# Kernel tuning notes

Measured on AMD Instinct MI355X. Metric: run time of the kernel, lower is better.

Reference implementation:

```python
import jax, jax.numpy as jnp
import numpy as np

B, T, N, E, H, L, K = 2, 32, 256, 1024, 16, 2, 256
MAXLEN = 512  # RelativeMultiheadAttention max_seq_len default
SCALES = (1, 2, 4)
TAU = 1.0


def setup_inputs() -> dict:
    key = jax.random.key(0)
    ks = jax.random.split(key, 9)
    s = 0.02
    A = 2 * L  # [layer0-spatial, layer0-temporal, layer1-spatial, layer1-temporal]
    return {
        "x": jax.random.normal(ks[0], (B, T, N, E), jnp.float32),
        "attn_wq": jax.random.normal(ks[1], (A, E, E), jnp.float32) * s,
        "attn_bq": jnp.zeros((A, E), jnp.float32),
        "attn_wk": jax.random.normal(ks[2], (A, E, E), jnp.float32) * s,
        "attn_bk": jnp.zeros((A, E), jnp.float32),
        "attn_wv": jax.random.normal(ks[3], (A, E, E), jnp.float32) * s,
        "attn_bv": jnp.zeros((A, E), jnp.float32),
        "attn_wd": jax.random.normal(ks[4], (A, E, E), jnp.float32) * s,
        "attn_bd": jnp.zeros((A, E), jnp.float32),
        "rel_bias": jax.random.normal(ks[5], (A, 2 * MAXLEN - 1, H), jnp.float32) * s,
        "sel_w": jax.random.normal(ks[6], (E, K), jnp.float32) * s,
        "sel_b": jnp.zeros((K,), jnp.float32),
    }


def _rel_attn(x, wq, bq, wk, bk, wv, bv, wd, bd, rb):
    # x: [Bx, S, E]; rb: [2*MAXLEN-1, H]
    Bx, S, _ = x.shape
    D = E // H
    q = (x @ wq + bq).reshape(Bx, S, H, D)
    k = (x @ wk + bk).reshape(Bx, S, H, D)
    v = (x @ wv + bv).reshape(Bx, S, H, D)
    scores = jnp.einsum('bshd,bthd->bhst', q, k) / jnp.sqrt(jnp.asarray(D, x.dtype))
    pos = jnp.arange(S)
    idx = pos[None, :] - pos[:, None] + (MAXLEN - 1)  # [S, S]
    bias = rb[idx]  # [S, S, H] gathered relative-position bias
    scores = scores + bias.transpose(2, 0, 1)[None]
    w = jax.nn.softmax(scores, axis=-1)
    ctx = jnp.einsum('bhst,bthd->bshd', w, v).reshape(Bx, S, E)
    return ctx @ wd + bd


def reference(x, attn_wq, attn_bq, attn_wk, attn_bk, attn_wv, attn_bv,
              attn_wd, attn_bd, rel_bias, sel_w, sel_b):
    h = x
    for l in range(L):
        # spatial attention over tokens within each frame
        i = 2 * l
        hs = h.reshape(B * T, N, E)
        hs = _rel_attn(hs, attn_wq[i], attn_bq[i], attn_wk[i], attn_bk[i],
                       attn_wv[i], attn_bv[i], attn_wd[i], attn_bd[i], rel_bias[i])
        # temporal attention across frames per spatial location
        j = 2 * l + 1
        ht = hs.reshape(B, T, N, E).transpose(0, 2, 1, 3).reshape(B * N, T, E)
        ht = _rel_attn(ht, attn_wq[j], attn_bq[j], attn_wk[j], attn_bk[j],
                       attn_wv[j], attn_bv[j], attn_wd[j], attn_bd[j], rel_bias[j])
        h = ht.reshape(B, N, T, E).transpose(0, 2, 1, 3)
    # DifferentiableTokenSelection: softmax-weighted pooling into K tokens
    flat = h.reshape(B, T * N, E)
    sc = flat @ sel_w + sel_b  # [B, T*N, K]
    wts = jax.nn.softmax(sc / TAU, axis=1)
    sel = jnp.einsum('bmk,bme->bke', wts, flat)  # [B, K, E]
    # multi-scale average pooling (kernel==stride==scale), concat along tokens
    outs = [sel.reshape(B, K // s, s, E).mean(axis=2) for s in SCALES]
    return jnp.concatenate(outs, axis=1)  # [B, K + K//2 + K//4, E]
```

## Files before the change

kernel.cpp:

```cpp
#include <hip/hip_runtime.h>
#include <stdint.h>


using f16x8 = __attribute__((ext_vector_type(8))) _Float16;
using f16x4 = __attribute__((ext_vector_type(4))) _Float16;
using f32x4 = __attribute__((ext_vector_type(4))) float;

__device__ __forceinline__ int tmap_dev(int m) {
    int bx = m >> 5;
    int s  = m & 31;
    int b  = bx >> 8;
    int n  = bx & 255;
    return (((b << 5) + s) << 8) + n;
}

__device__ __forceinline__ void load16(const _Float16* g, _Float16* l)
{
    __builtin_amdgcn_global_load_lds(
        (const __attribute__((address_space(1))) unsigned int*)g,
        (__attribute__((address_space(3))) unsigned int*)l,
        16, 0, 0);
}

__device__ __forceinline__ void split_f16(float v, _Float16& h, _Float16& l)
{
    h = (_Float16)v;
    l = (_Float16)(v - (float)h);
}

__global__ __launch_bounds__(256)
void conv_act(const float* __restrict__ src, _Float16* __restrict__ dh,
              _Float16* __restrict__ dl, int m_off)
{
    int idx = blockIdx.x * 256 + threadIdx.x;
    int e = idx << 3;
    int ml = e >> 10, col = e & 1023;
    const float* s = src + (size_t)(m_off + ml) * 1024 + col;
    float4 a = *(const float4*)s;
    float4 b = *(const float4*)(s + 4);
    float vv[8] = {a.x, a.y, a.z, a.w, b.x, b.y, b.z, b.w};
    f16x8 vh, vl;
    #pragma unroll
    for (int r = 0; r < 8; r++) {
        _Float16 h, l;
        split_f16(vv[r], h, l);
        vh[r] = h; vl[r] = l;
    }
    *(f16x8*)(dh + (size_t)ml * 1024 + col) = vh;
    *(f16x8*)(dl + (size_t)ml * 1024 + col) = vl;
}

__global__ __launch_bounds__(256)
void conv_wT(const float* __restrict__ W, _Float16* __restrict__ Th,
             _Float16* __restrict__ Tl, int ncols)
{
    __shared__ float Ls[64][65];
    const int n0 = blockIdx.x * 64, k0 = blockIdx.y * 64;
    const int t = threadIdx.x;
    const int kk = t >> 4, nn = (t & 15) << 2;
    #pragma unroll
    for (int i = 0; i < 4; i++) {
        float4 v = *(const float4*)(W + (size_t)(k0 + kk + 16 * i) * ncols + n0 + nn);
        Ls[kk + 16 * i][nn + 0] = v.x; Ls[kk + 16 * i][nn + 1] = v.y;
        Ls[kk + 16 * i][nn + 2] = v.z; Ls[kk + 16 * i][nn + 3] = v.w;
    }
    __syncthreads();
    const int nl = t >> 4, kc = (t & 15) << 2;
    #pragma unroll
    for (int i = 0; i < 4; i++) {
        int n = nl + 16 * i;
        f16x4 hh, ll;
        #pragma unroll
        for (int c = 0; c < 4; c++) {
            _Float16 h, l;
            split_f16(Ls[kc + c][n], h, l);
            hh[c] = h; ll[c] = l;
        }
        *(f16x4*)(Th + (size_t)(n0 + n) * 1024 + k0 + kc) = hh;
        *(f16x4*)(Tl + (size_t)(n0 + n) * 1024 + k0 + kc) = ll;
    }
}

template<int EPI>
__device__ __forceinline__ void gemm_core(
    const _Float16* __restrict__ Ah, const _Float16* __restrict__ Al,
    const _Float16* __restrict__ Wh, const _Float16* __restrict__ Wl,
    const float* __restrict__ bias,
    float* __restrict__ C, _Float16* __restrict__ Ch, _Float16* __restrict__ Cl,
    int ldc, int map_in, int m_off_in, int map_out, int m_off_out,
    int n0, int m0)
{
    __shared__ uint32_t smem_u[8512];
    _Float16* smem = (_Float16*)smem_u;
    _Float16* sAh = smem;
    _Float16* sAl = smem + 4096;
    _Float16* sBh = smem + 8192;
    _Float16* sBl = smem + 12288;

    const int tid = threadIdx.x;
    const int lane = tid & 63;
    const int wv = tid >> 6;
    const int fm = (wv >> 1) << 6;
    const int fn = (wv & 1) << 6;
    const int lm = lane & 15, lq = lane >> 4;

    f32x4 acc[4][4] = {};

    const int srow = tid >> 2;
    const int skc  = (tid & 3) << 3;
    const int gm0 = m_off_in + m0 + srow;
    const int gm1 = gm0 + 64;
    const int r0 = map_in ? tmap_dev(gm0) : gm0;
    const int r1 = map_in ? tmap_dev(gm1) : gm1;
    const _Float16* gAh0 = Ah + (size_t)r0 * 1024 + skc;
    const _Float16* gAh1 = Ah + (size_t)r1 * 1024 + skc;
    const _Float16* gAl0 = Al + (size_t)r0 * 1024 + skc;
    const _Float16* gAl1 = Al + (size_t)r1 * 1024 + skc;
    const _Float16* gB0 = Wh + (size_t)(n0 + srow) * 1024 + skc;
    const _Float16* gB1 = Wl + (size_t)(n0 + srow) * 1024 + skc;
    const int lo = tid << 3;

    for (int k0 = 0; k0 < 1024; k0 += 32) {
        load16(gAh0 + k0, sAh + lo);
        load16(gAh1 + k0, sAh + lo + 2048);
        load16(gAl0 + k0, sAl + lo);
        load16(gAl1 + k0, sAl + lo + 2048);
        load16(gB0 + k0,         sBh + lo);
        load16(gB0 + k0 + 65536, sBh + lo + 2048);
        load16(gB1 + k0,         sBl + lo);
        load16(gB1 + k0 + 65536, sBl + lo + 2048);
        __syncthreads();

        f16x8 ah[4], al[4], bh[4], bl[4];
        #pragma unroll
        for (int i = 0; i < 4; i++) {
            int ra = (fm + i * 16 + lm) * 32 + lq * 8;
            ah[i] = *(const f16x8*)(sAh + ra);
            al[i] = *(const f16x8*)(sAl + ra);
            int rb_ = (fn + i * 16 + lm) * 32 + lq * 8;
            bh[i] = *(const f16x8*)(sBh + rb_);
            bl[i] = *(const f16x8*)(sBl + rb_);
        }
        #pragma unroll
        for (int i = 0; i < 4; i++)
            #pragma unroll
            for (int j = 0; j < 4; j++) {
                acc[i][j] = __builtin_amdgcn_mfma_f32_16x16x32_f16(ah[i], bh[j], acc[i][j], 0, 0, 0);
                acc[i][j] = __builtin_amdgcn_mfma_f32_16x16x32_f16(ah[i], bl[j], acc[i][j], 0, 0, 0);
                acc[i][j] = __builtin_amdgcn_mfma_f32_16x16x32_f16(al[i], bh[j], acc[i][j], 0, 0, 0);
            }
        __syncthreads();
    }

    if (EPI == 0) {
        #pragma unroll
        for (int j = 0; j < 4; j++) {
            int n = n0 + fn + j * 16 + lm;
            float bb = bias[n];
            #pragma unroll
            for (int i = 0; i < 4; i++) {
                #pragma unroll
                for (int r = 0; r < 4; r++) {
                    int gm = m_off_out + m0 + fm + i * 16 + lq * 4 + r;
                    int row = map_out ? tmap_dev(gm) : gm;
                    C[(size_t)row * ldc + n] = acc[i][j][r] + bb;
                }
            }
        }
    }
}

__global__ __launch_bounds__(256, 2)
void gemm_f16s_f32(const _Float16* __restrict__ Ah, const _Float16* __restrict__ Al,
                   int map_in, int m_off_in,
                   const _Float16* __restrict__ Wh, const _Float16* __restrict__ Wl,
                   const float* __restrict__ bias, float* __restrict__ C, int ldc,
                   int map_out, int m_off_out)
{
    gemm_core<0>(Ah, Al, Wh, Wl, bias, C, nullptr, nullptr, ldc,
                 map_in, m_off_in, map_out, m_off_out,
                 blockIdx.x * 128, blockIdx.y * 128);
}

template<int EPI>
__device__ __forceinline__ void gemm256_core(
    uint32_t* __restrict__ smem_u,
    const _Float16* __restrict__ Ah, const _Float16* __restrict__ Al,
    const _Float16* __restrict__ Wh, const _Float16* __restrict__ Wl,
    const float* __restrict__ bias,
    _Float16* __restrict__ Ch, _Float16* __restrict__ Cl,
    int map_in, int m_off_in, int map_out, int m_off_out,
    int n0, int m0)
{
    _Float16* S = (_Float16*)smem_u;
    const int tid  = threadIdx.x;
    const int lane = tid & 63;
    const int wv = tid >> 6;
    const int wm = wv >> 1;
    const int fm = wm << 6;
    const int fn = (wv & 1) << 6;
    const int lm = lane & 15, lq = lane >> 4;
    const int ko = ((lq ^ ((lm >> 1) & 3)) << 3);

    f32x4 acc[4][4] = {};

    const int srow = tid >> 2;
    const int scol = (((tid & 3) ^ ((tid >> 3) & 3)) << 3);
    const int gm0 = m_off_in + m0 + srow;
    const int gm1 = gm0 + 128;
    const int r0 = map_in ? tmap_dev(gm0) : gm0;
    const int r1 = map_in ? tmap_dev(gm1) : gm1;
    const _Float16* gAh0 = Ah + (size_t)r0 * 1024 + scol;
    const _Float16* gAh1 = Ah + (size_t)r1 * 1024 + scol;
    const _Float16* gAl0 = Al + (size_t)r0 * 1024 + scol;
    const _Float16* gAl1 = Al + (size_t)r1 * 1024 + scol;
    const _Float16* gBh  = Wh + (size_t)(n0 + srow) * 1024 + scol;
    const _Float16* gBl  = Wl + (size_t)(n0 + srow) * 1024 + scol;
    const int lo = tid << 3;

    auto stage = [&](int t, int b) {
        const int k0 = t << 5;
        _Float16* d = S + b * 24576;
        load16(gAh0 + k0, d + lo);
        load16(gAh1 + k0, d + 4096  + lo);
        load16(gAl0 + k0, d + 8192  + lo);
        load16(gAl1 + k0, d + 12288 + lo);
        load16(gBh  + k0, d + 16384 + lo);
        load16(gBl  + k0, d + 20480 + lo);
    };

    auto ldfrags = [&](const _Float16* c,
                       f16x8 (&xah)[4], f16x8 (&xal)[4],
                       f16x8 (&xbh)[4], f16x8 (&xbl)[4]) {
        #pragma unroll
        for (int i = 0; i < 4; i++) {
            int ra = (fm + i * 16 + lm) * 32 + ko;
            xah[i] = *(const f16x8*)(c + ra);
            xal[i] = *(const f16x8*)(c + 8192 + ra);
            int rb = (fn + i * 16 + lm) * 32 + ko;
            xbh[i] = *(const f16x8*)(c + 16384 + rb);
            xbl[i] = *(const f16x8*)(c + 20480 + rb);
        }
    };

    f16x8 ahA[4], alA[4], bhA[4], blA[4];
    f16x8 ahB[4], alB[4], bhB[4], blB[4];

    auto kstep = [&](int t, int nxtbuf, int stagebuf,
                     f16x8 (&cah)[4], f16x8 (&cal)[4],
                     f16x8 (&cbh)[4], f16x8 (&cbl)[4],
                     f16x8 (&nah)[4], f16x8 (&nal)[4],
                     f16x8 (&nbh)[4], f16x8 (&nbl)[4],
                     bool prefetch, bool dostage) {
        if (prefetch) ldfrags(S + nxtbuf * 24576, nah, nal, nbh, nbl);
        if (dostage) stage(t + 2, stagebuf);
        __builtin_amdgcn_sched_barrier(0);
        __builtin_amdgcn_s_setprio(1);
        #pragma unroll
        for (int i = 0; i < 4; i++)
            #pragma unroll
            for (int j = 0; j < 4; j++) {
                acc[i][j] = __builtin_amdgcn_mfma_f32_16x16x32_f16(cah[i], cbh[j], acc[i][j], 0, 0, 0);
                acc[i][j] = __builtin_amdgcn_mfma_f32_16x16x32_f16(cah[i], cbl[j], acc[i][j], 0, 0, 0);
                acc[i][j] = __builtin_amdgcn_mfma_f32_16x16x32_f16(cal[i], cbh[j], acc[i][j], 0, 0, 0);
            }
        __builtin_amdgcn_s_setprio(0);
        asm volatile("s_waitcnt vmcnt(0)" ::: "memory");
        __builtin_amdgcn_s_barrier();
    };

    stage(0, 0);
    stage(1, 1);
    asm volatile("s_waitcnt vmcnt(0)" ::: "memory");
    __builtin_amdgcn_s_barrier();
    ldfrags(S, ahA, alA, bhA, blA);

    #pragma unroll 1
    for (int tt = 0; tt < 30; tt += 6) {
        kstep(tt + 0, 1, 2, ahA, alA, bhA, blA, ahB, alB, bhB, blB, true, true);
        kstep(tt + 1, 2, 0, ahB, alB, bhB, blB, ahA, alA, bhA, blA, true, true);
        kstep(tt + 2, 0, 1, ahA, alA, bhA, blA, ahB, alB, bhB, blB, true, true);
        kstep(tt + 3, 1, 2, ahB, alB, bhB, blB, ahA, alA, bhA, blA, true, true);
        kstep(tt + 4, 2, 0, ahA, alA, bhA, blA, ahB, alB, bhB, blB, true, true);
        kstep(tt + 5, 0, 1, ahB, alB, bhB, blB, ahA, alA, bhA, blA, true, true);
    }
    kstep(30, 1, 0, ahA, alA, bhA, blA, ahB, alB, bhB, blB, true,  false);
    kstep(31, 0, 0, ahB, alB, bhB, blB, ahA, alA, bhA, blA, false, false);

    if (EPI == 1) {
        #pragma unroll 1
        for (int q = 0; q < 4; q++) {
            __syncthreads();
            if (wm == q) {
                #pragma unroll
                for (int j = 0; j < 4; j++) {
                    int ncol = fn + j * 16 + lm;
                    float bb = bias[n0 + ncol];
                    #pragma unroll
                    for (int i = 0; i < 4; i++) {
                        #pragma unroll
                        for (int r = 0; r < 4; r++) {
                            float v = acc[i][j][r] + bb;
                            _Float16 h, l;
                            split_f16(v, h, l);
                            uint32_t ph = (uint32_t)__builtin_bit_cast(unsigned short, h);
                            uint32_t pl = (uint32_t)__builtin_bit_cast(unsigned short, l);
                            smem_u[(i * 16 + lq * 4 + r) * 132 + ncol] = ph | (pl << 16);
                        }
                    }
                }
            }
            __syncthreads();
            #pragma unroll
            for (int g = 0; g < 2; g++) {
                int u = tid + g * 512;
                int rl = u >> 4;
                int c8 = (u & 15) << 3;
                uint32_t p[8];
                #pragma unroll
                for (int x = 0; x < 8; x++) p[x] = smem_u[rl * 132 + c8 + x];
                f16x8 hh, ll;
                #pragma unroll
                for (int x = 0; x < 8; x++) {
                    hh[x] = __builtin_bit_cast(_Float16, (unsigned short)(p[x] & 0xffff));
                    ll[x] = __builtin_bit_cast(_Float16, (unsigned short)(p[x] >> 16));
                }
                int gm = m_off_out + m0 + q * 64 + rl;
                int row = map_out ? tmap_dev(gm) : gm;
                *(f16x8*)(Ch + (size_t)row * 1024 + n0 + c8) = hh;
                *(f16x8*)(Cl + (size_t)row * 1024 + n0 + c8) = ll;
            }
        }
    } else {
        #pragma unroll 1
        for (int q = 0; q < 4; q++) {
            __syncthreads();
            if (wm == q) {
                #pragma unroll
                for (int j = 0; j < 4; j++) {
                    int ncol = fn + j * 16 + lm;
                    float bb = bias[n0 + ncol];
                    #pragma unroll
                    for (int i = 0; i < 4; i++) {
                        #pragma unroll
                        for (int r = 0; r < 4; r++) {
                            float v = acc[i][j][r] + bb;
                            _Float16 h, l;
                            split_f16(v, h, l);
                            uint32_t ph = (uint32_t)__builtin_bit_cast(unsigned short, h);
                            uint32_t pl = (uint32_t)__builtin_bit_cast(unsigned short, l);
                            smem_u[(i * 16 + lq * 4 + r) * 129 + ncol] = ph | (pl << 16);
                        }
                    }
                }
            }
            __syncthreads();
            #pragma unroll
            for (int g = 0; g < 4; g++) {
                int u = tid + g * 512;
                int nn = u >> 4;
                int mg = (u & 15) << 2;
                uint32_t p0 = smem_u[(mg + 0) * 129 + nn];
                uint32_t p1 = smem_u[(mg + 1) * 129 + nn];
                uint32_t p2 = smem_u[(mg + 2) * 129 + nn];
                uint32_t p3 = smem_u[(mg + 3) * 129 + nn];
                f16x4 hh, ll;
                hh[0] = __builtin_bit_cast(_Float16, (unsigned short)(p0 & 0xffff));
                hh[1] = __builtin_bit_cast(_Float16, (unsigned short)(p1 & 0xffff));
                hh[2] = __builtin_bit_cast(_Float16, (unsigned short)(p2 & 0xffff));
                hh[3] = __builtin_bit_cast(_Float16, (unsigned short)(p3 & 0xffff));
                ll[0] = __builtin_bit_cast(_Float16, (unsigned short)(p0 >> 16));
                ll[1] = __builtin_bit_cast(_Float16, (unsigned short)(p1 >> 16));
                ll[2] = __builtin_bit_cast(_Float16, (unsigned short)(p2 >> 16));
                ll[3] = __builtin_bit_cast(_Float16, (unsigned short)(p3 >> 16));
                size_t off = (size_t)(n0 + nn) * 8192 + (m0 + q * 64 + mg);
                *(f16x4*)(Ch + off) = hh;
                *(f16x4*)(Cl + off) = ll;
            }
        }
    }
}

__global__ __launch_bounds__(512, 1)
void gemm_qkv256(const _Float16* __restrict__ Ah, const _Float16* __restrict__ Al,
                 int map_in, int m_off_in,
                 const _Float16* __restrict__ WTh, const _Float16* __restrict__ WTl,
                 const float* __restrict__ bq, const float* __restrict__ bk,
                 const float* __restrict__ bv,
                 _Float16* __restrict__ Qh, _Float16* __restrict__ Ql,
                 _Float16* __restrict__ Kh, _Float16* __restrict__ Kl,
                 _Float16* __restrict__ VTh, _Float16* __restrict__ VTl)
{
    __shared__ uint32_t smem_u[36864];
    const int bid = blockIdx.x;
    const int wg = (bid & 7) * 96 + (bid >> 3);
    const int z = wg >> 8;
    const int rem = wg & 255;
    const int m0 = (rem >> 3) << 8;
    const int n0 = (rem & 7) << 7;
    const _Float16* wh = WTh + (size_t)z * 1048576;
    const _Float16* wl = WTl + (size_t)z * 1048576;
    if (z < 2) {
        const float* bb = (z == 0) ? bq : bk;
        _Float16* oh = (z == 0) ? Qh : Kh;
        _Float16* ol = (z == 0) ? Ql : Kl;
        gemm256_core<1>(smem_u, Ah, Al, wh, wl, bb, oh, ol,
                        map_in, m_off_in, 0, 0, n0, m0);
    } else {
        gemm256_core<3>(smem_u, Ah, Al, wh, wl, bv, VTh, VTl,
                        map_in, m_off_in, 0, 0, n0, m0);
    }
}

__global__ __launch_bounds__(512, 1)
void gemm_h256(const _Float16* __restrict__ Ah, const _Float16* __restrict__ Al,
               int map_in, int m_off_in,
               const _Float16* __restrict__ Wh, const _Float16* __restrict__ Wl,
               const float* __restrict__ bias,
               _Float16* __restrict__ Ch, _Float16* __restrict__ Cl,
               int map_out, int m_off_out)
{
    __shared__ uint32_t smem_u[36864];
    const int bid = blockIdx.x;
    const int wg = (bid & 7) * 32 + (bid >> 3);
    const int m0 = (wg >> 3) << 8;
    const int n0 = (wg & 7) << 7;
    gemm256_core<1>(smem_u, Ah, Al, Wh, Wl, bias, Ch, Cl,
                    map_in, m_off_in, map_out, m_off_out, n0, m0);
}

__global__ __launch_bounds__(256, 2)
void attn_s_m(const _Float16* __restrict__ Qh, const _Float16* __restrict__ Ql,
              const _Float16* __restrict__ Kh, const _Float16* __restrict__ Kl,
              const _Float16* __restrict__ VTh, const _Float16* __restrict__ VTl,
              const float* __restrict__ RB,
              _Float16* __restrict__ Ch, _Float16* __restrict__ Cl)
{
    __shared__ _Float16 sKh[2048], sKl[2048];
    __shared__ _Float16 sVh[2560], sVl[2560];
    __shared__ _Float16 sPh[4][2560], sPl[4][2560];
    __shared__ float Bt[512];

    const int tid = threadIdx.x;
    const int lane = tid & 63;
    const int w = tid >> 6;
    const int lm = lane & 15, lq = lane >> 4;
    const int frame = blockIdx.x;
    const int h = blockIdx.y;
    const int rowbase = frame * 256;

    #pragma unroll
    for (int l = 0; l < 2; l++) {
        int idx = tid + l * 256;
        if (idx < 511) Bt[idx] = RB[(size_t)(256 + idx) * 16 + h];
    }

    f16x8 qbh[4][2], qbl[4][2];
    #pragma unroll
    for (int st = 0; st < 4; st++)
        #pragma unroll
        for (int kk = 0; kk < 2; kk++) {
            size_t qo = (size_t)(rowbase + w * 64 + st * 16 + lm) * 1024
                        + h * 64 + kk * 32 + lq * 8;
            qbh[st][kk] = *(const f16x8*)(Qh + qo);
            qbl[st][kk] = *(const f16x8*)(Ql + qo);
        }

    f32x4 cacc[4][4] = {};
    float lsum[4] = {0.f, 0.f, 0.f, 0.f};
    _Float16* Ph = sPh[w];
    _Float16* Pl = sPl[w];

    const int skrow = tid >> 3, skd = (tid & 7) << 3;
    const int svrow = tid >> 2, svj = (tid & 3) << 3;

    for (int jc = 0; jc < 8; jc++) {
        __syncthreads();
        {
            size_t ko = (size_t)(rowbase + jc * 32 + skrow) * 1024 + h * 64 + skd;
            *(f16x8*)(sKh + skrow * 64 + skd) = *(const f16x8*)(Kh + ko);
            *(f16x8*)(sKl + skrow * 64 + skd) = *(const f16x8*)(Kl + ko);
            size_t vo = (size_t)(h * 64 + svrow) * 8192 + rowbase + jc * 32 + svj;
            *(f16x8*)(sVh + svrow * 40 + svj) = *(const f16x8*)(VTh + vo);
            *(f16x8*)(sVl + svrow * 40 + svj) = *(const f16x8*)(VTl + vo);
        }
        __syncthreads();

        f32x4 sacc[2][4] = {};
        #pragma unroll
        for (int jt = 0; jt < 2; jt++) {
            f16x8 kah[2], kal[2];
            #pragma unroll
            for (int kk = 0; kk < 2; kk++) {
                int ra = (jt * 16 + lm) * 64 + kk * 32 + lq * 8;
                kah[kk] = *(const f16x8*)(sKh + ra);
                kal[kk] = *(const f16x8*)(sKl + ra);
            }
            #pragma unroll
            for (int st = 0; st < 4; st++)
                #pragma unroll
                for (int kk = 0; kk < 2; kk++) {
                    sacc[jt][st] = __builtin_amdgcn_mfma_f32_16x16x32_f16(kah[kk], qbh[st][kk], sacc[jt][st], 0, 0, 0);
                    sacc[jt][st] = __builtin_amdgcn_mfma_f32_16x16x32_f16(kah[kk], qbl[st][kk], sacc[jt][st], 0, 0, 0);
                    sacc[jt][st] = __builtin_amdgcn_mfma_f32_16x16x32_f16(kal[kk], qbh[st][kk], sacc[jt][st], 0, 0, 0);
                }
        }

        #pragma unroll
        for (int jt = 0; jt < 2; jt++)
            #pragma unroll
            for (int st = 0; st < 4; st++) {
                f16x4 p4h, p4l;
                #pragma unroll
                for (int r = 0; r < 4; r++) {
                    int j = jc * 32 + jt * 16 + lq * 4 + r;
                    int s = w * 64 + st * 16 + lm;
                    float p = __expf(sacc[jt][st][r] * 0.125f + Bt[j - s + 255]);
                    lsum[st] += p;
                    _Float16 hp, lp;
                    split_f16(p, hp, lp);
                    p4h[r] = hp; p4l[r] = lp;
                }
                int pa = (st * 16 + lm) * 40 + jt * 16 + lq * 4;
                *(f16x4*)(Ph + pa) = p4h;
                *(f16x4*)(Pl + pa) = p4l;
            }

        #pragma unroll
        for (int st = 0; st < 4; st++) {
            int pb = (st * 16 + lm) * 40 + lq * 8;
            f16x8 pbh = *(const f16x8*)(Ph + pb);
            f16x8 pbl = *(const f16x8*)(Pl + pb);
            #pragma unroll
            for (int dt = 0; dt < 4; dt++) {
                int va = (dt * 16 + lm) * 40 + lq * 8;
                f16x8 vah = *(const f16x8*)(sVh + va);
                f16x8 val = *(const f16x8*)(sVl + va);
                cacc[dt][st] = __builtin_amdgcn_mfma_f32_16x16x32_f16(vah, pbh, cacc[dt][st], 0, 0, 0);
                cacc[dt][st] = __builtin_amdgcn_mfma_f32_16x16x32_f16(vah, pbl, cacc[dt][st], 0, 0, 0);
                cacc[dt][st] = __builtin_amdgcn_mfma_f32_16x16x32_f16(val, pbh, cacc[dt][st], 0, 0, 0);
            }
        }
    }

    float inv[4];
    #pragma unroll
    for (int st = 0; st < 4; st++) {
        float t = lsum[st];
        t += __shfl_xor(t, 16);
        t += __shfl_xor(t, 32);
        inv[st] = 1.0f / t;
    }

    #pragma unroll
    for (int st = 0; st < 4; st++)
        #pragma unroll
        for (int dt = 0; dt < 4; dt++) {
            f16x4 oh, ol;
            #pragma unroll
            for (int r = 0; r < 4; r++) {
                _Float16 hp, lp;
                split_f16(cacc[dt][st][r] * inv[st], hp, lp);
                oh[r] = hp; ol[r] = lp;
            }
            size_t oo = (size_t)(rowbase + w * 64 + st * 16 + lm) * 1024
                        + h * 64 + dt * 16 + lq * 4;
            *(f16x4*)(Ch + oo) = oh;
            *(f16x4*)(Cl + oo) = ol;
        }
}

__global__ __launch_bounds__(256, 2)
void attn_t_m(const _Float16* __restrict__ Qh, const _Float16* __restrict__ Ql,
              const _Float16* __restrict__ Kh, const _Float16* __restrict__ Kl,
              const _Float16* __restrict__ VTh, const _Float16* __restrict__ VTl,
              const float* __restrict__ RB,
              _Float16* __restrict__ Ch, _Float16* __restrict__ Cl)
{
    __shared__ _Float16 sPh[4][1280], sPl[4][1280];
    __shared__ float Bt[64];

    const int tid = threadIdx.x;
    const int lane = tid & 63;
    const int w = tid >> 6;
    const int lm = lane & 15, lq = lane >> 4;
    const int h = blockIdx.y;
    const int bx = blockIdx.x * 4 + w;
    const int rowbase = bx * 32;

    if (tid < 63) Bt[tid] = RB[(size_t)(480 + tid) * 16 + h];
    __syncthreads();

    f16x8 qbh[2][2], qbl[2][2];
    #pragma unroll
    for (int st = 0; st < 2; st++)
        #pragma unroll
        for (int kk = 0; kk < 2; kk++) {
            size_t qo = (size_t)(rowbase + st * 16 + lm) * 1024 + h * 64 + kk * 32 + lq * 8;
            qbh[st][kk] = *(const f16x8*)(Qh + qo);
            qbl[st][kk] = *(const f16x8*)(Ql + qo);
        }

    f32x4 sacc[2][2] = {};
    #pragma unroll
    for (int jt = 0; jt < 2; jt++) {
        f16x8 kah[2], kal[2];
        #pragma unroll
        for (int kk = 0; kk < 2; kk++) {
            size_t ko = (size_t)(rowbase + jt * 16 + lm) * 1024 + h * 64 + kk * 32 + lq * 8;
            kah[kk] = *(const f16x8*)(Kh + ko);
            kal[kk] = *(const f16x8*)(Kl + ko);
        }
        #pragma unroll
        for (int st = 0; st < 2; st++)
            #pragma unroll
            for (int kk = 0; kk < 2; kk++) {
                sacc[jt][st] = __builtin_amdgcn_mfma_f32_16x16x32_f16(kah[kk], qbh[st][kk], sacc[jt][st], 0, 0, 0);
                sacc[jt][st] = __builtin_amdgcn_mfma_f32_16x16x32_f16(kah[kk], qbl[st][kk], sacc[jt][st], 0, 0, 0);
                sacc[jt][st] = __builtin_amdgcn_mfma_f32_16x16x32_f16(kal[kk], qbh[st][kk], sacc[jt][st], 0, 0, 0);
            }
    }

    float lsum[2] = {0.f, 0.f};
    _Float16* Ph = sPh[w];
    _Float16* Pl = sPl[w];
    #pragma unroll
    for (int jt = 0; jt < 2; jt++)
        #pragma unroll
        for (int st = 0; st < 2; st++) {
            f16x4 p4h, p4l;
            #pragma unroll
            for (int r = 0; r < 4; r++) {
                int j = jt * 16 + lq * 4 + r;
                int s = st * 16 + lm;
                float p = __expf(sacc[jt][st][r] * 0.125f + Bt[j - s + 31]);
                lsum[st] += p;
                _Float16 hp, lp;
                split_f16(p, hp, lp);
                p4h[r] = hp; p4l[r] = lp;
            }
            int pa = (st * 16 + lm) * 40 + jt * 16 + lq * 4;
            *(f16x4*)(Ph + pa) = p4h;
            *(f16x4*)(Pl + pa) = p4l;
        }

    f16x8 vah[4], val[4];
    #pragma unroll
    for (int dt = 0; dt < 4; dt++) {
        size_t vo = (size_t)(h * 64 + dt * 16 + lm) * 8192 + rowbase + lq * 8;
        vah[dt] = *(const f16x8*)(VTh + vo);
        val[dt] = *(const f16x8*)(VTl + vo);
    }
    f32x4 cacc[4][2] = {};
    #pragma unroll
    for (int st = 0; st < 2; st++) {
        int pb = (st * 16 + lm) * 40 + lq * 8;
        f16x8 pbh = *(const f16x8*)(Ph + pb);
        f16x8 pbl = *(const f16x8*)(Pl + pb);
        #pragma unroll
        for (int dt = 0; dt < 4; dt++) {
            cacc[dt][st] = __builtin_amdgcn_mfma_f32_16x16x32_f16(vah[dt], pbh, cacc[dt][st], 0, 0, 0);
            cacc[dt][st] = __builtin_amdgcn_mfma_f32_16x16x32_f16(vah[dt], pbl, cacc[dt][st], 0, 0, 0);
            cacc[dt][st] = __builtin_amdgcn_mfma_f32_16x16x32_f16(val[dt], pbh, cacc[dt][st], 0, 0, 0);
        }
    }

    float inv[2];
    #pragma unroll
    for (int st = 0; st < 2; st++) {
        float t = lsum[st];
        t += __shfl_xor(t, 16);
        t += __shfl_xor(t, 32);
        inv[st] = 1.0f / t;
    }

    #pragma unroll
    for (int st = 0; st < 2; st++)
        #pragma unroll
        for (int dt = 0; dt < 4; dt++) {
            f16x4 oh, ol;
            #pragma unroll
            for (int r = 0; r < 4; r++) {
                _Float16 hp, lp;
                split_f16(cacc[dt][st][r] * inv[st], hp, lp);
                oh[r] = hp; ol[r] = lp;
            }
            size_t oo = (size_t)(rowbase + st * 16 + lm) * 1024 + h * 64 + dt * 16 + lq * 4;
            *(f16x4*)(Ch + oo) = oh;
            *(f16x4*)(Cl + oo) = ol;
        }
}

__global__ __launch_bounds__(256)
void colsum_part_kernel(const float* __restrict__ SC, float* __restrict__ P)
{
    int bid = blockIdx.x;
    int b = bid >> 7, chunk = bid & 127;
    int base = b * 8192 + chunk * 64;
    int k = threadIdx.x;
    float sum = 0.0f;
    for (int r = 0; r < 64; r++)
        sum += __expf(SC[(size_t)(base + r) * 256 + k]);
    P[(size_t)bid * 256 + k] = sum;
}

__global__ __launch_bounds__(256)
void colsum_reduce_kernel(const float* __restrict__ P, float* __restrict__ CS)
{
    int b = blockIdx.x;
    int k = threadIdx.x;
    float s = 0.0f;
    for (int c = 0; c < 128; c++)
        s += P[(size_t)(b * 128 + c) * 256 + k];
    CS[b * 256 + k] = s;
}

__global__ __launch_bounds__(256)
void trans_wts(const float* __restrict__ SC, const float* __restrict__ CS,
               _Float16* __restrict__ Th, _Float16* __restrict__ Tl)
{
    __shared__ float L[64][65];
    const int mt = blockIdx.x * 64;
    const int kt = blockIdx.y * 64;
    const int b  = mt >> 13;
    const int ml = mt & 8191;
    const int tid = threadIdx.x;
    #pragma unroll
    for (int l = 0; l < 4; l++) {
        int idx = tid + 256 * l;
        int r = idx >> 4, c4 = (idx & 15) << 2;
        float4 v = *(const float4*)(SC + (size_t)(mt + r) * 256 + kt + c4);
        L[r][c4 + 0] = __expf(v.x); L[r][c4 + 1] = __expf(v.y);
        L[r][c4 + 2] = __expf(v.z); L[r][c4 + 3] = __expf(v.w);
    }
    __syncthreads();
    #pragma unroll
    for (int l = 0; l < 4; l++) {
        int idx = tid + 256 * l;
        int rk = idx >> 4, c4 = (idx & 15) << 2;
        float inv = 1.0f / CS[b * 256 + kt + rk];
        f16x4 hh, ll;
        #pragma unroll
        for (int u = 0; u < 4; u++) {
            _Float16 h, l2;
            split_f16(L[c4 + u][rk] * inv, h, l2);
            hh[u] = h; ll[u] = l2;
        }
        size_t o = ((size_t)b * 256 + kt + rk) * 8192 + ml + c4;
        *(f16x4*)(Th + o) = hh;
        *(f16x4*)(Tl + o) = ll;
    }
}

__global__ __launch_bounds__(256)
void trans_f16(const _Float16* __restrict__ Sh, const _Float16* __restrict__ Sl,
               _Float16* __restrict__ Th, _Float16* __restrict__ Tl)
{
    __shared__ _Float16 L[64][72];
    const int mt = blockIdx.x * 64, et = blockIdx.y * 64;
    const _Float16* S = blockIdx.z ? Sl : Sh;
    _Float16* T = blockIdx.z ? Tl : Th;
    const int tid = threadIdx.x;
    #pragma unroll
    for (int l = 0; l < 2; l++) {
        int v = tid * 2 + l;
        int r = v >> 3, c8 = (v & 7) << 3;
        *(f16x8*)&L[r][c8] = *(const f16x8*)(S + (size_t)(mt + r) * 1024 + et + c8);
    }
    __syncthreads();
    #pragma unroll
    for (int l = 0; l < 2; l++) {
        int v = tid * 2 + l;
        int r = v >> 3, c8 = (v & 7) << 3;
        f16x8 o;
        #pragma unroll
        for (int u = 0; u < 8; u++) o[u] = L[c8 + u][r];
        *(f16x8*)(T + (size_t)(et + r) * 16384 + mt + c8) = o;
    }
}

__global__ __launch_bounds__(256, 2)
void gemm_selm(const _Float16* __restrict__ Wth, const _Float16* __restrict__ Wtl,
               const _Float16* __restrict__ Hth, const _Float16* __restrict__ Htl,
               float* __restrict__ P)
{
    __shared__ _Float16 sAh[4096], sAl[4096], sBh[4096], sBl[4096];
    const int tid = threadIdx.x;
    const int lane = tid & 63;
    const int wv = tid >> 6;
    const int fm = (wv >> 1) << 6;
    const int fn = (wv & 1) << 6;
    const int lm = lane & 15, lq = lane >> 4;
    const int n0 = blockIdx.x * 128;
    const int m0 = blockIdx.y * 128;
    const int z  = blockIdx.z;
    const int b = z >> 3, sp = z & 7;

    f32x4 acc[4][4] = {};

    const int srow = tid >> 2;
    const int skc  = (tid & 3) << 3;
    const _Float16* gAh0 = Wth + ((size_t)b * 256 + m0 + srow) * 8192 + sp * 1024 + skc;
    const _Float16* gAl0 = Wtl + ((size_t)b * 256 + m0 + srow) * 8192 + sp * 1024 + skc;
    const _Float16* gB0 = Hth + (size_t)(n0 + srow) * 16384 + b * 8192 + sp * 1024 + skc;
    const _Float16* gB1 = Htl + (size_t)(n0 + srow) * 16384 + b * 8192 + sp * 1024 + skc;
    const int lo = tid << 3;

    for (int k0 = 0; k0 < 1024; k0 += 32) {
        load16(gAh0 + k0,          sAh + lo);
        load16(gAh0 + k0 + 524288, sAh + lo + 2048);
        load16(gAl0 + k0,          sAl + lo);
        load16(gAl0 + k0 + 524288, sAl + lo + 2048);
        load16(gB0 + k0,           sBh + lo);
        load16(gB0 + k0 + 1048576, sBh + lo + 2048);
        load16(gB1 + k0,           sBl + lo);
        load16(gB1 + k0 + 1048576, sBl + lo + 2048);
        __syncthreads();

        f16x8 ah[4], al[4], bh[4], bl[4];
        #pragma unroll
        for (int i = 0; i < 4; i++) {
            int ra = (fm + i * 16 + lm) * 32 + lq * 8;
            ah[i] = *(const f16x8*)(sAh + ra);
            al[i] = *(const f16x8*)(sAl + ra);
            int rb_ = (fn + i * 16 + lm) * 32 + lq * 8;
            bh[i] = *(const f16x8*)(sBh + rb_);
            bl[i] = *(const f16x8*)(sBl + rb_);
        }
        #pragma unroll
        for (int i = 0; i < 4; i++)
            #pragma unroll
            for (int j = 0; j < 4; j++) {
                acc[i][j] = __builtin_amdgcn_mfma_f32_16x16x32_f16(ah[i], bh[j], acc[i][j], 0, 0, 0);
                acc[i][j] = __builtin_amdgcn_mfma_f32_16x16x32_f16(ah[i], bl[j], acc[i][j], 0, 0, 0);
                acc[i][j] = __builtin_amdgcn_mfma_f32_16x16x32_f16(al[i], bh[j], acc[i][j], 0, 0, 0);
            }
        __syncthreads();
    }

    float* Pz = P + (size_t)z * 262144;
    #pragma unroll
    for (int j = 0; j < 4; j++) {
        int n = n0 + fn + j * 16 + lm;
        #pragma unroll
        for (int i = 0; i < 4; i++)
            #pragma unroll
            for (int r = 0; r < 4; r++) {
                int k = m0 + fm + i * 16 + lq * 4 + r;
                Pz[(size_t)k * 1024 + n] = acc[i][j][r];
            }
    }
}

__global__ __launch_bounds__(256)
void sel_reduce(const float* __restrict__ P, float* __restrict__ SEL)
{
    int idx4 = blockIdx.x * 256 + threadIdx.x;
    int e = idx4 << 2;
    int b = e >> 18;
    int rest = e & 262143;
    const float* p = P + (size_t)(b * 8) * 262144 + rest;
    float4 acc = {0.f, 0.f, 0.f, 0.f};
    #pragma unroll
    for (int s = 0; s < 8; s++) {
        float4 v = *(const float4*)(p + (size_t)s * 262144);
        acc.x += v.x; acc.y += v.y; acc.z += v.z; acc.w += v.w;
    }
    *(float4*)(SEL + e) = acc;
}

__global__ __launch_bounds__(256)
void pool_kernel(const float* __restrict__ SEL, float* __restrict__ out)
{
    int i4 = blockIdx.x * 256 + threadIdx.x;
    int e  = i4 << 2;
    int row = e >> 10;
    int b = row / 448;
    int r = row - b * 448;
    int c = e & 1023;
    const float* sb = SEL + (size_t)b * (256 * 1024);
    float4 o;
    if (r < 256) {
        o = *(const float4*)(sb + (size_t)r * 1024 + c);
    } else if (r < 384) {
        int r2 = (r - 256) * 2;
        float4 x0 = *(const float4*)(sb + (size_t)r2 * 1024 + c);
        float4 x1 = *(const float4*)(sb + (size_t)(r2 + 1) * 1024 + c);
        o.x = 0.5f * (x0.x + x1.x); o.y = 0.5f * (x0.y + x1.y);
        o.z = 0.5f * (x0.z + x1.z); o.w = 0.5f * (x0.w + x1.w);
    } else {
        int r4 = (r - 384) * 4;
        float4 x0 = *(const float4*)(sb + (size_t)(r4 + 0) * 1024 + c);
        float4 x1 = *(const float4*)(sb + (size_t)(r4 + 1) * 1024 + c);
        float4 x2 = *(const float4*)(sb + (size_t)(r4 + 2) * 1024 + c);
        float4 x3 = *(const float4*)(sb + (size_t)(r4 + 3) * 1024 + c);
        o.x = 0.25f * (x0.x + x1.x + x2.x + x3.x);
        o.y = 0.25f * (x0.y + x1.y + x2.y + x3.y);
        o.z = 0.25f * (x0.z + x1.z + x2.z + x3.z);
        o.w = 0.25f * (x0.w + x1.w + x2.w + x3.w);
    }
    *(float4*)(out + e) = o;
}

extern "C" void kernel_launch(void* const* d_in, const int* in_sizes, int n_in,
                              void* d_out, int out_size, void* d_ws, size_t ws_size,
                              hipStream_t stream)
{
    const float* x    = (const float*)d_in[0];
    const float* wq   = (const float*)d_in[1];
    const float* bq   = (const float*)d_in[2];
    const float* wk   = (const float*)d_in[3];
    const float* bk   = (const float*)d_in[4];
    const float* wv   = (const float*)d_in[5];
    const float* bv   = (const float*)d_in[6];
    const float* wd   = (const float*)d_in[7];
    const float* bd   = (const float*)d_in[8];
    const float* rb   = (const float*)d_in[9];
    const float* selw = (const float*)d_in[10];
    const float* selb = (const float*)d_in[11];
    float* out = (float*)d_out;

    float* base = (float*)d_ws;
    _Float16* Hh  = (_Float16*)base;
    _Float16* Hl  = Hh + 16777216;
    _Float16* Qh  = (_Float16*)(base + 16777216);
    _Float16* Ql  = Qh + 8388608;
    _Float16* Kh  = Ql + 8388608;
    _Float16* Kl  = Kh + 8388608;
    _Float16* VTh = (_Float16*)(base + 33554432);
    _Float16* VTl = VTh + 8388608;
    _Float16* CXh = (_Float16*)(base + 41943040);
    _Float16* CXl = CXh + 8388608;
    _Float16* WTh = (_Float16*)(base + 50331648);
    _Float16* WTl = WTh + 4194304;
    _Float16* Ah  = (_Float16*)(base + 54525952);
    _Float16* Al  = Ah + 8388608;
    float* SC   = (float*)Qh;
    float* Pp   = (float*)Kh;
    float* SEL  = (float*)Kl;
    float* PART = SEL + 524288;
    float* CSUM = PART + 65536;
    _Float16* WTTh = CXh;
    _Float16* WTTl = CXl;
    _Float16* HTh  = Ah;
    _Float16* HTl  = VTh;

    const dim3 blk(256);
    const dim3 blk2(512);

    for (int a = 0; a < 4; a++) {
        const int mi = (a & 1);
        const size_t wo = (size_t)a * 1048576;
        const int bo = a * 1024;
        const float* rba = rb + (size_t)a * 1023 * 16;

        conv_wT<<<dim3(16, 16), blk, 0, stream>>>(wq + wo, WTh,           WTl,           1024);
        conv_wT<<<dim3(16, 16), blk, 0, stream>>>(wk + wo, WTh + 1048576, WTl + 1048576, 1024);
        conv_wT<<<dim3(16, 16), blk, 0, stream>>>(wv + wo, WTh + 2097152, WTl + 2097152, 1024);
        conv_wT<<<dim3(16, 16), blk, 0, stream>>>(wd + wo, WTh + 3145728, WTl + 3145728, 1024);

        for (int c = 0; c < 2; c++) {
            const int mo = c * 8192;
            const _Float16 *sH, *sL;
            int sm, so;
            if (a == 0) {
                conv_act<<<4096, blk, 0, stream>>>(x, Ah, Al, mo);
                sH = Ah; sL = Al; sm = 0; so = 0;
            } else {
                sH = Hh; sL = Hl; sm = mi; so = mo;
            }
            gemm_qkv256<<<dim3(768), blk2, 0, stream>>>(
                sH, sL, sm, so, WTh, WTl, bq + bo, bk + bo, bv + bo,
                Qh, Ql, Kh, Kl, VTh, VTl);
            if (mi == 0)
                attn_s_m<<<dim3(32, 16), blk, 0, stream>>>(Qh, Ql, Kh, Kl, VTh, VTl, rba, CXh, CXl);
            else
                attn_t_m<<<dim3(64, 16), blk, 0, stream>>>(Qh, Ql, Kh, Kl, VTh, VTl, rba, CXh, CXl);
            gemm_h256<<<dim3(256), blk2, 0, stream>>>(
                CXh, CXl, 0, 0, WTh + 3145728, WTl + 3145728, bd + bo, Hh, Hl, mi, mo);
        }
    }

    conv_wT<<<dim3(4, 16), blk, 0, stream>>>(selw, WTh, WTl, 256);
    gemm_f16s_f32<<<dim3(2, 128), blk, 0, stream>>>(
        Hh, Hl, 0, 0, WTh, WTl, selb, SC, 256, 0, 0);
    colsum_part_kernel<<<256, blk, 0, stream>>>(SC, PART);
    colsum_reduce_kernel<<<2, blk, 0, stream>>>(PART, CSUM);
    trans_wts<<<dim3(256, 4), blk, 0, stream>>>(SC, CSUM, WTTh, WTTl);
    trans_f16<<<dim3(256, 16, 2), blk, 0, stream>>>(Hh, Hl, HTh, HTl);
    gemm_selm<<<dim3(8, 2, 16), blk, 0, stream>>>(WTTh, WTTl, HTh, HTl, Pp);
    sel_reduce<<<512, blk, 0, stream>>>(Pp, SEL);
    pool_kernel<<<896, blk, 0, stream>>>(SEL, out);
}
```

Measured before the change: 2.368 ms.

## Load A-low fragments from global directly and double-buffer smaller LDS in 256-tile GEMM

The 256-row split-f16 GEMM no longer stages the A low-half tile through LDS. Each lane instead reads its A-low MFMA fragment straight from global memory inside the k-step. The pipeline moves from triple buffering with register-prefetched fragments to a simpler double-buffered LDS scheme, shrinking shared memory from about 144KB to 64KB. Launch bounds are raised to 4 blocks per CU to raise occupancy. The risks are register pressure and spilling from the tighter launch bound, less latency hiding, and uncached per-lane global loads sitting on the MFMA critical path.

Result: slower. 3.039 ms (+28.3%).

```diff
diff --git a/kernel.cpp b/kernel.cpp
--- a/kernel.cpp
+++ b/kernel.cpp
@@ -86,16 +86,11 @@
     const _Float16* __restrict__ Ah, const _Float16* __restrict__ Al,
     const _Float16* __restrict__ Wh, const _Float16* __restrict__ Wl,
     const float* __restrict__ bias,
-    float* __restrict__ C, _Float16* __restrict__ Ch, _Float16* __restrict__ Cl,
-    int ldc, int map_in, int m_off_in, int map_out, int m_off_out,
+    float* __restrict__ C, int ldc,
+    int map_in, int m_off_in, int map_out, int m_off_out,
     int n0, int m0)
 {
-    __shared__ uint32_t smem_u[8512];
-    _Float16* smem = (_Float16*)smem_u;
-    _Float16* sAh = smem;
-    _Float16* sAl = smem + 4096;
-    _Float16* sBh = smem + 8192;
-    _Float16* sBl = smem + 12288;
+    __shared__ _Float16 sAh[4096], sAl[4096], sBh[4096], sBl[4096];
 
     const int tid = threadIdx.x;
     const int lane = tid & 63;
@@ -177,9 +172,39 @@
                    const float* __restrict__ bias, float* __restrict__ C, int ldc,
                    int map_out, int m_off_out)
 {
-    gemm_core<0>(Ah, Al, Wh, Wl, bias, C, nullptr, nullptr, ldc,
+    gemm_core<0>(Ah, Al, Wh, Wl, bias, C, ldc,
                  map_in, m_off_in, map_out, m_off_out,
                  blockIdx.x * 128, blockIdx.y * 128);
+}
+
+#define MMI(T, CBUF, II, PAL)                                                    \
+{                                                                                \
+    f16x8 fah = *(const f16x8*)((CBUF) + (fm + (II) * 16 + lm) * 32 + ko);       \
+    f16x8 fal = *(const f16x8*)((PAL) + ((T) << 5));                             \
+    _Pragma("unroll")                                                            \
+    for (int j = 0; j < 4; j++) {                                                \
+        acc[II][j] = __builtin_amdgcn_mfma_f32_16x16x32_f16(fah, fbh[j], acc[II][j], 0, 0, 0); \
+        acc[II][j] = __builtin_amdgcn_mfma_f32_16x16x32_f16(fah, fbl[j], acc[II][j], 0, 0, 0); \
+        acc[II][j] = __builtin_amdgcn_mfma_f32_16x16x32_f16(fal, fbh[j], acc[II][j], 0, 0, 0); \
+    }                                                                            \
+}
+
+#define KSTEP(T, CUR, DOSTAGE)                                                   \
+{                                                                                \
+    if (DOSTAGE) stage((T) + 1, (CUR) ^ 1);                                      \
+    const _Float16* cbuf = S + (CUR) * 16384;                                    \
+    f16x8 fbh[4], fbl[4];                                                        \
+    _Pragma("unroll")                                                            \
+    for (int j = 0; j < 4; j++) {                                                \
+        fbh[j] = *(const f16x8*)(cbuf + 8192  + (fn + j * 16 + lm) * 32 + ko);   \
+        fbl[j] = *(const f16x8*)(cbuf + 12288 + (fn + j * 16 + lm) * 32 + ko);   \
+    }                                                                            \
+    MMI(T, cbuf, 0, pAl0)                                                        \
+    MMI(T, cbuf, 1, pAl1)                                                        \
+    MMI(T, cbuf, 2, pAl2)                                                        \
+    MMI(T, cbuf, 3, pAl3)                                                        \
+    asm volatile("s_waitcnt vmcnt(0) lgkmcnt(0)" ::: "memory");                  \
+    __builtin_amdgcn_s_barrier();                                                \
 }
 
 template<int EPI>
@@ -212,80 +237,38 @@
     const int r1 = map_in ? tmap_dev(gm1) : gm1;
     const _Float16* gAh0 = Ah + (size_t)r0 * 1024 + scol;
     const _Float16* gAh1 = Ah + (size_t)r1 * 1024 + scol;
-    const _Float16* gAl0 = Al + (size_t)r0 * 1024 + scol;
-    const _Float16* gAl1 = Al + (size_t)r1 * 1024 + scol;
     const _Float16* gBh  = Wh + (size_t)(n0 + srow) * 1024 + scol;
     const _Float16* gBl  = Wl + (size_t)(n0 + srow) * 1024 + scol;
     const int lo = tid << 3;
 
+    const int gmf = m_off_in + m0 + fm + lm;
+    const int rA0 = map_in ? tmap_dev(gmf +  0) : (gmf +  0);
+    const int rA1 = map_in ? tmap_dev(gmf + 16) : (gmf + 16);
+    const int rA2 = map_in ? tmap_dev(gmf + 32) : (gmf + 32);
+    const int rA3 = map_in ? tmap_dev(gmf + 48) : (gmf + 48);
+    const _Float16* pAl0 = Al + (size_t)rA0 * 1024 + (lq << 3);
+    const _Float16* pAl1 = Al + (size_t)rA1 * 1024 + (lq << 3);
+    const _Float16* pAl2 = Al + (size_t)rA2 * 1024 + (lq << 3);
+    const _Float16* pAl3 = Al + (size_t)rA3 * 1024 + (lq << 3);
+
     auto stage = [&](int t, int b) {
         const int k0 = t << 5;
-        _Float16* d = S + b * 24576;
+        _Float16* d = S + b * 16384;
         load16(gAh0 + k0, d + lo);
         load16(gAh1 + k0, d + 4096  + lo);
-        load16(gAl0 + k0, d + 8192  + lo);
-        load16(gAl1 + k0, d + 12288 + lo);
-        load16(gBh  + k0, d + 16384 + lo);
-        load16(gBl  + k0, d + 20480 + lo);
+        load16(gBh  + k0, d + 8192  + lo);
+        load16(gBl  + k0, d + 12288 + lo);
     };
 
-    auto ldfrags = [&](const _Float16* c,
-                       f16x8 (&xah)[4], f16x8 (&xal)[4],
-                       f16x8 (&xbh)[4], f16x8 (&xbl)[4]) {
-        #pragma unroll
-        for (int i = 0; i < 4; i++) {
-            int ra = (fm + i * 16 + lm) * 32 + ko;
-            xah[i] = *(const f16x8*)(c + ra);
-            xal[i] = *(const f16x8*)(c + 8192 + ra);
-            int rb = (fn + i * 16 + lm) * 32 + ko;
-            xbh[i] = *(const f16x8*)(c + 16384 + rb);
-            xbl[i] = *(const f16x8*)(c + 20480 + rb);
-        }
-    };
-
-    f16x8 ahA[4], alA[4], bhA[4], blA[4];
-    f16x8 ahB[4], alB[4], bhB[4], blB[4];
-
-    auto kstep = [&](int t, int nxtbuf, int stagebuf,
-                     f16x8 (&cah)[4], f16x8 (&cal)[4],
-                     f16x8 (&cbh)[4], f16x8 (&cbl)[4],
-                     f16x8 (&nah)[4], f16x8 (&nal)[4],
-                     f16x8 (&nbh)[4], f16x8 (&nbl)[4],
-                     bool prefetch, bool dostage) {
-        if (prefetch) ldfrags(S + nxtbuf * 24576, nah, nal, nbh, nbl);
-        if (dostage) stage(t + 2, stagebuf);
-        __builtin_amdgcn_sched_barrier(0);
-        __builtin_amdgcn_s_setprio(1);
-        #pragma unroll
-        for (int i = 0; i < 4; i++)
-            #pragma unroll
-            for (int j = 0; j < 4; j++) {
-                acc[i][j] = __builtin_amdgcn_mfma_f32_16x16x32_f16(cah[i], cbh[j], acc[i][j], 0, 0, 0);
-                acc[i][j] = __builtin_amdgcn_mfma_f32_16x16x32_f16(cah[i], cbl[j], acc[i][j], 0, 0, 0);
-                acc[i][j] = __builtin_amdgcn_mfma_f32_16x16x32_f16(cal[i], cbh[j], acc[i][j], 0, 0, 0);
-            }
-        __builtin_amdgcn_s_setprio(0);
-        asm volatile("s_waitcnt vmcnt(0)" ::: "memory");
-        __builtin_amdgcn_s_barrier();
-    };
-
     stage(0, 0);
-    stage(1, 1);
     asm volatile("s_waitcnt vmcnt(0)" ::: "memory");
     __builtin_amdgcn_s_barrier();
-    ldfrags(S, ahA, alA, bhA, blA);
 
     #pragma unroll 1
-    for (int tt = 0; tt < 30; tt += 6) {
-        kstep(tt + 0, 1, 2, ahA, alA, bhA, blA, ahB, alB, bhB, blB, true, true);
-        kstep(tt + 1, 2, 0, ahB, alB, bhB, blB, ahA, alA, bhA, blA, true, true);
-        kstep(tt + 2, 0, 1, ahA, alA, bhA, blA, ahB, alB, bhB, blB, true, true);
-        kstep(tt + 3, 1, 2, ahB, alB, bhB, blB, ahA, alA, bhA, blA, true, true);
-        kstep(tt + 4, 2, 0, ahA, alA, bhA, blA, ahB, alB, bhB, blB, true, true);
-        kstep(tt + 5, 0, 1, ahB, alB, bhB, blB, ahA, alA, bhA, blA, true, true);
-    }
-    kstep(30, 1, 0, ahA, alA, bhA, blA, ahB, alB, bhB, blB, true,  false);
-    kstep(31, 0, 0, ahB, alB, bhB, blB, ahA, alA, bhA, blA, false, false);
+    for (int tt = 0; tt < 32; tt += 2) {
+        KSTEP(tt,     0, (tt < 31))
+        KSTEP(tt + 1, 1, (tt + 2 < 32))
+    }
 
     if (EPI == 1) {
         #pragma unroll 1
@@ -381,7 +364,10 @@
     }
 }
 
-__global__ __launch_bounds__(512, 1)
+#undef MMI
+#undef KSTEP
+
+__global__ __launch_bounds__(512, 4)
 void gemm_qkv256(const _Float16* __restrict__ Ah, const _Float16* __restrict__ Al,
                  int map_in, int m_off_in,
                  const _Float16* __restrict__ WTh, const _Float16* __restrict__ WTl,
@@ -391,7 +377,7 @@
                  _Float16* __restrict__ Kh, _Float16* __restrict__ Kl,
                  _Float16* __restrict__ VTh, _Float16* __restrict__ VTl)
 {
-    __shared__ uint32_t smem_u[36864];
+    __shared__ uint32_t smem_u[16384];
     const int bid = blockIdx.x;
     const int wg = (bid & 7) * 96 + (bid >> 3);
     const int z = wg >> 8;
@@ -412,7 +398,7 @@
     }
 }
 
-__global__ __launch_bounds__(512, 1)
+__global__ __launch_bounds__(512, 4)
 void gemm_h256(const _Float16* __restrict__ Ah, const _Float16* __restrict__ Al,
                int map_in, int m_off_in,
                const _Float16* __restrict__ Wh, const _Float16* __restrict__ Wl,
@@ -420,7 +406,7 @@
                _Float16* __restrict__ Ch, _Float16* __restrict__ Cl,
                int map_out, int m_off_out)
 {
-    __shared__ uint32_t smem_u[36864];
+    __shared__ uint32_t smem_u[16384];
     const int bid = blockIdx.x;
     const int wg = (bid & 7) * 32 + (bid >> 3);
     const int m0 = (wg >> 3) << 8;
```
